# Optimization experiments

Hardware: AMD Instinct MI355X
Metric: run time of the kernel (lower is better)

## Reference

```python
import jax, jax.numpy as jnp
import numpy as np

B = 256          # batch
MID = 16384      # mid_siz
OUT = 16384      # out_siz
C = 16           # channel_siz
NLVL = 8         # nlvl (== klvl here since floor(log2(OUT/2))=13 >= 8)
MIDF = MID >> NLVL   # mid_filter_siz = 64
OUTF = OUT >> NLVL   # out_filter_siz = 64
NB = 1 << NLVL       # 256 leaf branches
STD = 0.5


def setup_inputs() -> dict:
    key = jax.random.key(0)
    ks = jax.random.split(key, 6)
    in_data = jax.random.normal(ks[0], (B, MID, 2), jnp.float32)
    # learned parameters (buildRand: normal(0, 0.5) filters, zero biases)
    mid_dense = jax.random.normal(ks[1], (1, MID, 2), jnp.float32) * STD
    in_filter = jax.random.normal(ks[2], (MIDF, 1, C), jnp.float32) * STD   # conv1d [width,in,out]
    in_bias = jnp.zeros((C,), jnp.float32)
    # level lvl (1..NLVL) uses filters[lvl-1, :2**lvl]; padded to NB branches
    filters = jax.random.normal(ks[3], (NLVL, NB, 2, C, C), jnp.float32) * STD
    biases = jnp.zeros((NLVL, NB, C), jnp.float32)
    fea_dense = jax.random.normal(ks[4], (NB, C, OUTF), jnp.float32) * STD
    return dict(in_data=in_data, mid_dense=mid_dense, in_filter=in_filter,
                in_bias=in_bias, filters=filters, biases=biases, fea_dense=fea_dense)


def reference(in_data, mid_dense, in_filter, in_bias, filters, biases, fea_dense):
    # elementwise modulation then split real/imag channels: (B, 2, MID)
    x = jnp.moveaxis(in_data * mid_dense, -1, 1)
    # level-0 conv1d: kernel MIDF, stride MIDF//2 -> overlapping half-windows.
    # Split signal into half-width chunks h; window t = [h[t], h[t+1]].
    half = MIDF // 2
    h = x.reshape(B, 2, MID // half, half)                 # (B,2,512,32)
    W1 = in_filter[:half, 0, :]                            # (32,C)
    W2 = in_filter[half:, 0, :]
    s = jnp.einsum('bisw,wc->bisc', h[:, :, :-1], W1) \
        + jnp.einsum('bisw,wc->bisc', h[:, :, 1:], W2)
    s = jax.nn.relu(s + in_bias)                           # (B,2,2^(n+1)-1,C)
    state = s[:, :, None]                                  # (B,2,nb=1,L,C)
    # butterfly tree: each level doubles branches; conv kernel=2, stride=2, VALID
    for lvl in range(1, NLVL + 1):
        nb = 1 << lvl
        p = jnp.repeat(state, 2, axis=2)                   # child itk <- parent itk//2
        L = p.shape[3]                                     # odd: 2^(n+1-lvl+1)-1
        xw = p[:, :, :, :L - 1, :].reshape(B, 2, nb, (L - 1) // 2, 2, C)
        W = filters[lvl - 1, :nb]                          # (nb,2,C,C)
        bb = biases[lvl - 1, :nb]                          # (nb,C)
        state = jax.nn.relu(
            jnp.einsum('bintkc,nkcd->bintd', xw, W) + bb[None, None, :, None, :])
    feat = state[:, :, :, 0, :]                            # (B,2,NB,C): L==1 at last level
    outp = jnp.einsum('binc,ncf->binf', feat, fea_dense)   # per-branch dense projection
    R = outp[:, 0].reshape(B, OUT // 2, 2)
    I = outp[:, 1].reshape(B, OUT // 2, 2)
    out_data = ((R[:, :, 0] - I[:, :, 1]) / MID).reshape(B, OUT // 2, 1)
    return out_data, R[:, :, 1]
```

## Files before the change

kernel.cpp:

```cpp
#include <hip/hip_runtime.h>
#include <hip/hip_bf16.h>


#define OUT_HALF 2097152

typedef __attribute__((ext_vector_type(4))) float f32x4;
typedef __attribute__((ext_vector_type(8))) short s16x8;

__device__ __forceinline__ uint fsw(uint a) {
    return a ^ ((((a >> 6) ^ (a >> 8)) & 3u) << 4);
}
__device__ __forceinline__ ushort bfr(float f) {
    __hip_bfloat16 h = __float2bfloat16(f);
    union { __hip_bfloat16 h; ushort u; } cv; cv.h = h; return cv.u;
}
__device__ __forceinline__ uint pk(float a, float b) {
    return (uint)bfr(a) | ((uint)bfr(b) << 16);
}

__device__ __forceinline__ void tree_level(
    char* smb, const int lane, const int wave,
    uint AOff, uint NOff, int lgR, int lgNP, int nTiles,
    uint WOff, int wnb, uint LBOff, int bnb)
{
    const int m  = lane & 15;
    const int kg = lane >> 4;
    const int lgTPP = lgR - 4;
    for (int at = wave; at < nTiles; at += 4) {
        const int p  = at >> lgTPP;
        const int tc = at & ((1 << lgTPP) - 1);
        const int np = p & ((1 << lgNP) - 1);
        const int ii = p >> lgNP;
        s16x8 af = *(const s16x8*)(smb + AOff + (p << (lgR + 6)) +
                                   fsw((uint)((tc * 16 + m) * 64 + kg * 16)));
#pragma unroll
        for (int sib = 0; sib < 2; sib++) {
            const int nl = 2 * np + sib;
            s16x8 bf = *(const s16x8*)(smb + WOff +
                         fsw((uint)((wnb + nl) * 1024 + m * 64 + kg * 16)));
            float bv = *(const float*)(smb + LBOff + ((bnb + nl) * 16 + m) * 4);
            f32x4 acc = {bv, bv, bv, bv};
            acc = __builtin_amdgcn_mfma_f32_16x16x32_bf16(af, bf, acc, 0, 0, 0);
            const int p2 = (ii << (lgNP + 1)) + nl;
            const uint wb = NOff + (p2 << (lgR + 5));
            const int r2 = tc * 8 + kg * 2;
            *(uint*)(smb + wb + fsw((uint)(r2 * 64 + m * 4))) =
                pk(fmaxf(acc.x, 0.f), fmaxf(acc.y, 0.f));
            *(uint*)(smb + wb + fsw((uint)((r2 + 1) * 64 + m * 4))) =
                pk(fmaxf(acc.z, 0.f), fmaxf(acc.w, 0.f));
        }
    }
}

__global__ __launch_bounds__(256, 4)
void ibf_A(const float* __restrict__ in_data, const float* __restrict__ mid_dense,
           const float* __restrict__ in_filter, const float* __restrict__ in_bias,
           const float* __restrict__ filters, const float* __restrict__ biases,
           uint* __restrict__ S3)
{
    __shared__ __align__(16) char smb[29760];
    const int tid = threadIdx.x, lane = tid & 63, wave = tid >> 6;
    const int b = blockIdx.x;
    const int th = blockIdx.y >> 1;
    const int i  = blockIdx.y & 1;

    {
        const float4* inb = (const float4*)in_data + (size_t)b * 8192 + th * 2048;
        const float4* mdb = (const float4*)mid_dense + th * 2048;
        for (int mp = tid; mp < 2064; mp += 256) {
            float4 iv = inb[mp], mv = mdb[mp];
            float xa = i ? iv.y * mv.y : iv.x * mv.x;
            float xb = i ? iv.w * mv.w : iv.z * mv.z;
            *(uint*)(smb + fsw((uint)(mp * 4))) = pk(xa, xb);
        }
    }
    for (int t = tid; t < 3584; t += 256) {
        int nidx = t >> 8, r = t & 255, d = r & 15, c = r >> 4;
        int lvl = (nidx < 2) ? 1 : ((nidx < 6) ? 2 : 3);
        int n = nidx - ((1 << lvl) - 2);
        const float* src = filters + (size_t)(lvl - 1) * 131072 + n * 512 + c * 16 + d;
        *(uint*)(smb + 12416 + fsw((uint)(nidx * 1024 + d * 64 + c * 4))) = pk(src[0], src[256]);
    }
    for (int t = tid; t < 512; t += 256) {
        int c = t >> 5, w2 = t & 31;
        *(uint*)(smb + 26752 + fsw((uint)(c * 128 + w2 * 4))) =
            pk(in_filter[(2 * w2) * 16 + c], in_filter[(2 * w2 + 1) * 16 + c]);
    }
    if (tid < 240) {
        float v;
        if (tid < 224) {
            int nidx = tid >> 4;
            int lvl = (nidx < 2) ? 1 : ((nidx < 6) ? 2 : 3);
            int n = nidx - ((1 << lvl) - 2);
            v = biases[(size_t)(lvl - 1) * 4096 + n * 16 + (tid & 15)];
        } else v = in_bias[tid - 224];
        *(float*)(smb + 28800 + tid * 4) = v;
    }
    __syncthreads();

    {
        const int m = lane & 15, kg = lane >> 4;
        s16x8 b0 = *(const s16x8*)(smb + 26752 + fsw((uint)(m * 128 + kg * 16)));
        s16x8 b1 = *(const s16x8*)(smb + 26752 + fsw((uint)(m * 128 + 64 + kg * 16)));
        float bv = *(const float*)(smb + 28800 + (224 + m) * 4);
        for (int at = wave; at < 8; at += 4) {
            int tc = at;
            s16x8 a0 = *(const s16x8*)(smb + fsw((uint)((tc * 16 + m) * 64 + kg * 16)));
            s16x8 a1 = *(const s16x8*)(smb + fsw((uint)((tc * 16 + m) * 64 + 64 + kg * 16)));
            f32x4 acc = {bv, bv, bv, bv};
            acc = __builtin_amdgcn_mfma_f32_16x16x32_bf16(a0, b0, acc, 0, 0, 0);
            acc = __builtin_amdgcn_mfma_f32_16x16x32_bf16(a1, b1, acc, 0, 0, 0);
            int r2 = tc * 8 + kg * 2;
            *(uint*)(smb + 8320 + fsw((uint)(r2 * 64 + m * 4))) =
                pk(fmaxf(acc.x, 0.f), fmaxf(acc.y, 0.f));
            *(uint*)(smb + 8320 + fsw((uint)((r2 + 1) * 64 + m * 4))) =
                pk(fmaxf(acc.z, 0.f), fmaxf(acc.w, 0.f));
        }
    }
    __syncthreads();
    tree_level(smb, lane, wave, 8320, 0,    6, 0, 4, 12416, 0, 28800, 0);
    __syncthreads();
    tree_level(smb, lane, wave, 0,    8320, 5, 1, 4, 12416, 2, 28800, 2);
    __syncthreads();
    {
        const int m = lane & 15, kg = lane >> 4;
        for (int at = wave; at < 4; at += 4) {
            s16x8 af = *(const s16x8*)(smb + 8320 + (at << 10) + fsw((uint)(m * 64 + kg * 16)));
#pragma unroll
            for (int sib = 0; sib < 2; sib++) {
                int n3 = 2 * at + sib;
                s16x8 bf = *(const s16x8*)(smb + 12416 +
                             fsw((uint)((6 + n3) * 1024 + m * 64 + kg * 16)));
                float bv = *(const float*)(smb + 28800 + ((6 + n3) * 16 + m) * 4);
                f32x4 acc = {bv, bv, bv, bv};
                acc = __builtin_amdgcn_mfma_f32_16x16x32_bf16(af, bf, acc, 0, 0, 0);
                int bi = 2 * b + i;
                int t4 = th * 8 + kg * 2;
                uint idx = ((uint)(n3 * 512 + bi) * 16 + t4) * 16 + m;
                S3[idx]      = pk(fmaxf(acc.x, 0.f), fmaxf(acc.y, 0.f));
                S3[idx + 16] = pk(fmaxf(acc.z, 0.f), fmaxf(acc.w, 0.f));
            }
        }
    }
}

__global__ __launch_bounds__(256, 2)
void ibf_BC(const float* __restrict__ filters, const float* __restrict__ biases,
            const float* __restrict__ fea_dense, const uint* __restrict__ S3,
            float* __restrict__ out)
{
    __shared__ __align__(16) char smb[33536];
    const int tid = threadIdx.x, lane = tid & 63, wave = tid >> 6;
    const int n3 = blockIdx.x, chunk = blockIdx.y;
    const int m = lane & 15, kg = lane >> 4;

    for (int o = tid * 16; o < 16384; o += 4096)
        *(float4*)(smb + 16384 + o) = make_float4(0.f, 0.f, 0.f, 0.f);

    const float* FB1 = filters + (size_t)3 * 131072 + ((size_t)(n3 << 1)) * 512;
    const float* FB2 = filters + (size_t)4 * 131072 + ((size_t)(n3 << 2)) * 512;
    const float* FB3 = filters + (size_t)5 * 131072 + ((size_t)(n3 << 3)) * 512;
    const float* FB4 = filters + (size_t)6 * 131072 + ((size_t)(n3 << 4)) * 512;
    const float* FB5 = filters + (size_t)7 * 131072 + ((size_t)(n3 << 5)) * 512;
    const float* BB1 = biases + (size_t)3 * 4096 + (n3 << 1) * 16;
    const float* BB2 = biases + (size_t)4 * 4096 + (n3 << 2) * 16;
    const float* BB3 = biases + (size_t)5 * 4096 + (n3 << 3) * 16;
    const float* BB4 = biases + (size_t)6 * 4096 + (n3 << 4) * 16;
    const float* BB5 = biases + (size_t)7 * 4096 + (n3 << 5) * 16;

#define LDFRAG(dst, fb, nl)                                                  \
    {                                                                        \
        const float* s_ = (fb) + (nl) * 512 + m;                             \
        _Pragma("unroll")                                                    \
        for (int c4 = 0; c4 < 4; c4++) {                                     \
            int c_ = kg * 4 + c4;                                            \
            (&(dst).x)[c4] = pk(s_[c_ * 16], s_[256 + c_ * 16]);             \
        }                                                                    \
    }

    uint4 f4[2], f5[4];
    float b4[2], b5[4];
    LDFRAG(f4[0], FB1, 0); LDFRAG(f4[1], FB1, 1);
    b4[0] = BB1[m]; b4[1] = BB1[16 + m];
#pragma unroll
    for (int s = 0; s < 4; s++) { LDFRAG(f5[s], FB2, s); b5[s] = BB2[s * 16 + m]; }
    {
        const char* src = (const char*)S3 + ((size_t)n3 * 512 + chunk * 8) * 1024;
        for (int ci = tid; ci < 512; ci += 256)
            *(float4*)(smb + fsw((uint)(ci * 16))) = *(const float4*)(src + ci * 16);
    }
    __syncthreads();

    uint4 f6[4];
    float b6[4];
    {
        const int n0 = (wave >> 1) * 2;
        LDFRAG(f6[0], FB3, n0);     b6[0] = BB3[(n0) * 16 + m];
        LDFRAG(f6[1], FB3, n0 + 1); b6[1] = BB3[(n0 + 1) * 16 + m];
        LDFRAG(f6[2], FB3, n0 + 4); b6[2] = BB3[(n0 + 4) * 16 + m];
        LDFRAG(f6[3], FB3, n0 + 5); b6[3] = BB3[(n0 + 5) * 16 + m];
    }
#pragma unroll
    for (int t2 = 0; t2 < 2; t2++) {
        const int tc = wave + t2 * 4;
        s16x8 af = *(const s16x8*)(smb + fsw((uint)((tc * 16 + m) * 64 + kg * 16)));
#pragma unroll
        for (int sib = 0; sib < 2; sib++) {
            f32x4 acc = {b4[sib], b4[sib], b4[sib], b4[sib]};
            acc = __builtin_amdgcn_mfma_f32_16x16x32_bf16(af, *(const s16x8*)&f4[sib], acc, 0, 0, 0);
            const uint wb = 8192u + (uint)sib * 4096u;
            const int r2 = tc * 8 + kg * 2;
            *(uint*)(smb + wb + fsw((uint)(r2 * 64 + m * 4))) = pk(fmaxf(acc.x, 0.f), fmaxf(acc.y, 0.f));
            *(uint*)(smb + wb + fsw((uint)((r2 + 1) * 64 + m * 4))) = pk(fmaxf(acc.z, 0.f), fmaxf(acc.w, 0.f));
        }
    }
    __syncthreads();

    uint4 f7[4];
    float b7[4];
    {
        LDFRAG(f7[0], FB4, 2 * wave);     b7[0] = BB4[(2 * wave) * 16 + m];
        LDFRAG(f7[1], FB4, 2 * wave + 1); b7[1] = BB4[(2 * wave + 1) * 16 + m];
        LDFRAG(f7[2], FB4, 2 * wave + 8); b7[2] = BB4[(2 * wave + 8) * 16 + m];
        LDFRAG(f7[3], FB4, 2 * wave + 9); b7[3] = BB4[(2 * wave + 9) * 16 + m];
    }
#pragma unroll
    for (int t2 = 0; t2 < 2; t2++) {
        const int at = wave + t2 * 4;
        const int p = at >> 2, tc = at & 3;
        s16x8 af = *(const s16x8*)(smb + 8192 + p * 4096 + fsw((uint)((tc * 16 + m) * 64 + kg * 16)));
#pragma unroll
        for (int sib = 0; sib < 2; sib++) {
            const int nl = 2 * p + sib;
            f32x4 acc = {b5[nl], b5[nl], b5[nl], b5[nl]};
            acc = __builtin_amdgcn_mfma_f32_16x16x32_bf16(af, *(const s16x8*)&f5[nl], acc, 0, 0, 0);
            const uint wb = (uint)nl * 2048u;
            const int r2 = tc * 8 + kg * 2;
            *(uint*)(smb + wb + fsw((uint)(r2 * 64 + m * 4))) = pk(fmaxf(acc.x, 0.f), fmaxf(acc.y, 0.f));
            *(uint*)(smb + wb + fsw((uint)((r2 + 1) * 64 + m * 4))) = pk(fmaxf(acc.z, 0.f), fmaxf(acc.w, 0.f));
        }
    }
    __syncthreads();

    uint4 f8[8];
    float b8[8];
#pragma unroll
    for (int t4 = 0; t4 < 4; t4++) {
        const int at = wave + 4 * t4;
        LDFRAG(f8[2 * t4],     FB5, 2 * at);     b8[2 * t4]     = BB5[(2 * at) * 16 + m];
        LDFRAG(f8[2 * t4 + 1], FB5, 2 * at + 1); b8[2 * t4 + 1] = BB5[(2 * at + 1) * 16 + m];
    }
#pragma unroll
    for (int t2 = 0; t2 < 2; t2++) {
        const int at = wave + t2 * 4;
        const int p = at >> 1, tc = at & 1;
        s16x8 af = *(const s16x8*)(smb + p * 2048 + fsw((uint)((tc * 16 + m) * 64 + kg * 16)));
#pragma unroll
        for (int sib = 0; sib < 2; sib++) {
            const int nl = 2 * p + sib;
            const int fi = t2 * 2 + sib;
            f32x4 acc = {b6[fi], b6[fi], b6[fi], b6[fi]};
            acc = __builtin_amdgcn_mfma_f32_16x16x32_bf16(af, *(const s16x8*)&f6[fi], acc, 0, 0, 0);
            const uint wb = 8192u + (uint)nl * 1024u;
            const int r2 = tc * 8 + kg * 2;
            *(uint*)(smb + wb + fsw((uint)(r2 * 64 + m * 4))) = pk(fmaxf(acc.x, 0.f), fmaxf(acc.y, 0.f));
            *(uint*)(smb + wb + fsw((uint)((r2 + 1) * 64 + m * 4))) = pk(fmaxf(acc.z, 0.f), fmaxf(acc.w, 0.f));
        }
    }
    __syncthreads();

#pragma unroll
    for (int t2 = 0; t2 < 2; t2++) {
        const int p = wave + t2 * 4;
        s16x8 af = *(const s16x8*)(smb + 8192 + p * 1024 + fsw((uint)(m * 64 + kg * 16)));
#pragma unroll
        for (int sib = 0; sib < 2; sib++) {
            const int nl = 2 * p + sib;
            const int fi = t2 * 2 + sib;
            f32x4 acc = {b7[fi], b7[fi], b7[fi], b7[fi]};
            acc = __builtin_amdgcn_mfma_f32_16x16x32_bf16(af, *(const s16x8*)&f7[fi], acc, 0, 0, 0);
            const uint wb = (uint)nl * 512u;
            const int r2 = kg * 2;
            *(uint*)(smb + wb + fsw((uint)(r2 * 64 + m * 4))) = pk(fmaxf(acc.x, 0.f), fmaxf(acc.y, 0.f));
            *(uint*)(smb + wb + fsw((uint)((r2 + 1) * 64 + m * 4))) = pk(fmaxf(acc.z, 0.f), fmaxf(acc.w, 0.f));
        }
    }
    __syncthreads();

#pragma unroll
    for (int t4 = 0; t4 < 4; t4++) {
        const int at = wave + 4 * t4;
        s16x8 af = *(const s16x8*)(smb + at * 512 + fsw((uint)(m * 64 + kg * 16)));
#pragma unroll
        for (int sib = 0; sib < 2; sib++) {
            const int nl = 2 * at + sib;
            const int fi = t4 * 2 + sib;
            f32x4 acc = {b8[fi], b8[fi], b8[fi], b8[fi]};
            acc = __builtin_amdgcn_mfma_f32_16x16x32_bf16(af, *(const s16x8*)&f8[fi], acc, 0, 0, 0);
            if (kg < 2) {
                float v[4] = {fmaxf(acc.x, 0.f), fmaxf(acc.y, 0.f),
                              fmaxf(acc.z, 0.f), fmaxf(acc.w, 0.f)};
#pragma unroll
                for (int j = 0; j < 4; j++) {
                    uint o = (uint)(nl * 512 + (kg * 4 + j) * 64 + m * 2);
                    *(ushort*)(smb + 16384 + fsw(o)) = bfr(v[j]);
                }
            }
        }
    }
    __syncthreads();

    for (int q = 0; q < 8; q++) {
        int n8l = wave * 8 + q;
        int gn8 = n3 * 32 + n8l;
        s16x8 af = *(const s16x8*)(smb + 16384 +
                     fsw((uint)(n8l * 512 + m * 64 + kg * 16)));
        const float* fb = fea_dense + (size_t)gn8 * 1024;
#pragma unroll
        for (int ut = 0; ut < 4; ut++) {
            s16x8 bf = {0, 0, 0, 0, 0, 0, 0, 0};
            if (kg < 2) {
                const float* fp = fb + kg * 512 + ut * 16 + m;
                bf[0] = (short)bfr(fp[0]);   bf[1] = (short)bfr(fp[64]);
                bf[2] = (short)bfr(fp[128]); bf[3] = (short)bfr(fp[192]);
                bf[4] = (short)bfr(fp[256]); bf[5] = (short)bfr(fp[320]);
                bf[6] = (short)bfr(fp[384]); bf[7] = (short)bfr(fp[448]);
            }
            f32x4 acc = {0.f, 0.f, 0.f, 0.f};
            acc = __builtin_amdgcn_mfma_f32_16x16x32_bf16(af, bf, acc, 0, 0, 0);
            float s0 = __shfl_xor(acc.y, 1);
            float s2 = __shfl_xor(acc.w, 1);
            if (kg < 2) {
                int g = gn8 * 32 + ut * 8 + (m >> 1);
                bool odd = (m & 1);
                float v0 = odd ? acc.x : (acc.x - s0) * (1.f / 16384.f);
                float v1 = odd ? acc.z : (acc.z - s2) * (1.f / 16384.f);
                size_t off = (odd ? (size_t)OUT_HALF : (size_t)0) + (size_t)g;
                int b0 = chunk * 4 + kg * 2;
                out[(size_t)b0 * 8192 + off]       = v0;
                out[(size_t)(b0 + 1) * 8192 + off] = v1;
            }
        }
    }
#undef LDFRAG
}

extern "C" void kernel_launch(void* const* d_in, const int* in_sizes, int n_in,
                              void* d_out, int out_size, void* d_ws, size_t ws_size,
                              hipStream_t stream) {
    const float* in_data   = (const float*)d_in[0];
    const float* mid_dense = (const float*)d_in[1];
    const float* in_filter = (const float*)d_in[2];
    const float* in_bias   = (const float*)d_in[3];
    const float* filters   = (const float*)d_in[4];
    const float* biases    = (const float*)d_in[5];
    const float* fea_dense = (const float*)d_in[6];
    float* out = (float*)d_out;
    uint* S3   = (uint*)d_ws;

    ibf_A<<<dim3(256, 4), 256, 0, stream>>>(in_data, mid_dense, in_filter, in_bias,
                                            filters, biases, S3);
    ibf_BC<<<dim3(8, 64), 256, 0, stream>>>(filters, biases, fea_dense, S3, out);
}
```

Baseline: 40.70 us.

## Vectorize filter staging, prefetch fea_dense in registers, reorder S3 load, use dynamic LDS

Filter staging in the first kernel now loads float4 vectors and packs four bf16 pairs per thread instead of scalar gathers. In the second kernel, the S3 tile copy is issued first. The final projection double-buffers fea_dense values in registers so global loads for the next branch overlap the current MFMA work. Shared memory becomes a dynamically sized extern buffer. This raises register pressure, since 64 floats are prefetched per lane, which may hurt occupancy.

```diff
diff --git a/kernel.cpp b/kernel.cpp
--- a/kernel.cpp
+++ b/kernel.cpp
@@ -6,6 +6,8 @@
 
 typedef __attribute__((ext_vector_type(4))) float f32x4;
 typedef __attribute__((ext_vector_type(8))) short s16x8;
+
+extern __shared__ char smb[];
 
 __device__ __forceinline__ uint fsw(uint a) {
     return a ^ ((((a >> 6) ^ (a >> 8)) & 3u) << 4);
@@ -19,7 +21,7 @@
 }
 
 __device__ __forceinline__ void tree_level(
-    char* smb, const int lane, const int wave,
+    const int lane, const int wave,
     uint AOff, uint NOff, int lgR, int lgNP, int nTiles,
     uint WOff, int wnb, uint LBOff, int bnb)
 {
@@ -58,7 +60,6 @@
            const float* __restrict__ filters, const float* __restrict__ biases,
            uint* __restrict__ S3)
 {
-    __shared__ __align__(16) char smb[29760];
     const int tid = threadIdx.x, lane = tid & 63, wave = tid >> 6;
     const int b = blockIdx.x;
     const int th = blockIdx.y >> 1;
@@ -74,12 +75,20 @@
             *(uint*)(smb + fsw((uint)(mp * 4))) = pk(xa, xb);
         }
     }
-    for (int t = tid; t < 3584; t += 256) {
-        int nidx = t >> 8, r = t & 255, d = r & 15, c = r >> 4;
+    for (int t = tid; t < 896; t += 256) {
+        int nidx = t >> 6, r = t & 63, c = r >> 2, d4 = (r & 3) * 4;
         int lvl = (nidx < 2) ? 1 : ((nidx < 6) ? 2 : 3);
         int n = nidx - ((1 << lvl) - 2);
-        const float* src = filters + (size_t)(lvl - 1) * 131072 + n * 512 + c * 16 + d;
-        *(uint*)(smb + 12416 + fsw((uint)(nidx * 1024 + d * 64 + c * 4))) = pk(src[0], src[256]);
+        const float* src = filters + (size_t)(lvl - 1) * 131072 + n * 512 + c * 16 + d4;
+        float4 v0 = *(const float4*)(src);
+        float4 v1 = *(const float4*)(src + 256);
+        const float* p0 = &v0.x;
+        const float* p1 = &v1.x;
+#pragma unroll
+        for (int j = 0; j < 4; j++) {
+            *(uint*)(smb + 12416 + fsw((uint)(nidx * 1024 + (d4 + j) * 64 + c * 4))) =
+                pk(p0[j], p1[j]);
+        }
     }
     for (int t = tid; t < 512; t += 256) {
         int c = t >> 5, w2 = t & 31;
@@ -118,9 +127,9 @@
         }
     }
     __syncthreads();
-    tree_level(smb, lane, wave, 8320, 0,    6, 0, 4, 12416, 0, 28800, 0);
-    __syncthreads();
-    tree_level(smb, lane, wave, 0,    8320, 5, 1, 4, 12416, 2, 28800, 2);
+    tree_level(lane, wave, 8320, 0,    6, 0, 4, 12416, 0, 28800, 0);
+    __syncthreads();
+    tree_level(lane, wave, 0,    8320, 5, 1, 4, 12416, 2, 28800, 2);
     __syncthreads();
     {
         const int m = lane & 15, kg = lane >> 4;
@@ -149,11 +158,15 @@
             const float* __restrict__ fea_dense, const uint* __restrict__ S3,
             float* __restrict__ out)
 {
-    __shared__ __align__(16) char smb[33536];
     const int tid = threadIdx.x, lane = tid & 63, wave = tid >> 6;
     const int n3 = blockIdx.x, chunk = blockIdx.y;
     const int m = lane & 15, kg = lane >> 4;
 
+    {
+        const char* src = (const char*)S3 + ((size_t)n3 * 512 + chunk * 8) * 1024;
+        for (int ci = tid; ci < 512; ci += 256)
+            *(float4*)(smb + fsw((uint)(ci * 16))) = *(const float4*)(src + ci * 16);
+    }
     for (int o = tid * 16; o < 16384; o += 4096)
         *(float4*)(smb + 16384 + o) = make_float4(0.f, 0.f, 0.f, 0.f);
 
@@ -184,11 +197,6 @@
     b4[0] = BB1[m]; b4[1] = BB1[16 + m];
 #pragma unroll
     for (int s = 0; s < 4; s++) { LDFRAG(f5[s], FB2, s); b5[s] = BB2[s * 16 + m]; }
-    {
-        const char* src = (const char*)S3 + ((size_t)n3 * 512 + chunk * 8) * 1024;
-        for (int ci = tid; ci < 512; ci += 256)
-            *(float4*)(smb + fsw((uint)(ci * 16))) = *(const float4*)(src + ci * 16);
-    }
     __syncthreads();
 
     uint4 f6[4];
@@ -310,35 +318,54 @@
     }
     __syncthreads();
 
-    for (int q = 0; q < 8; q++) {
-        int n8l = wave * 8 + q;
-        int gn8 = n3 * 32 + n8l;
-        s16x8 af = *(const s16x8*)(smb + 16384 +
-                     fsw((uint)(n8l * 512 + m * 64 + kg * 16)));
-        const float* fb = fea_dense + (size_t)gn8 * 1024;
-#pragma unroll
-        for (int ut = 0; ut < 4; ut++) {
-            s16x8 bf = {0, 0, 0, 0, 0, 0, 0, 0};
-            if (kg < 2) {
-                const float* fp = fb + kg * 512 + ut * 16 + m;
-                bf[0] = (short)bfr(fp[0]);   bf[1] = (short)bfr(fp[64]);
-                bf[2] = (short)bfr(fp[128]); bf[3] = (short)bfr(fp[192]);
-                bf[4] = (short)bfr(fp[256]); bf[5] = (short)bfr(fp[320]);
-                bf[6] = (short)bfr(fp[384]); bf[7] = (short)bfr(fp[448]);
+    {
+        float feA[32], feB[32];
+        const float* fbase = fea_dense + (size_t)(n3 * 32 + wave * 8) * 1024 + kg * 512 + m;
+        if (kg < 2) {
+#pragma unroll
+            for (int ut = 0; ut < 4; ut++)
+#pragma unroll
+                for (int j = 0; j < 8; j++)
+                    feA[ut * 8 + j] = fbase[ut * 16 + j * 64];
+        }
+#pragma unroll
+        for (int q = 0; q < 8; q++) {
+            float* cur = (q & 1) ? feB : feA;
+            float* nxt = (q & 1) ? feA : feB;
+            if (q < 7 && kg < 2) {
+                const float* fn = fbase + (size_t)(q + 1) * 1024;
+#pragma unroll
+                for (int ut = 0; ut < 4; ut++)
+#pragma unroll
+                    for (int j = 0; j < 8; j++)
+                        nxt[ut * 8 + j] = fn[ut * 16 + j * 64];
             }
-            f32x4 acc = {0.f, 0.f, 0.f, 0.f};
-            acc = __builtin_amdgcn_mfma_f32_16x16x32_bf16(af, bf, acc, 0, 0, 0);
-            float s0 = __shfl_xor(acc.y, 1);
-            float s2 = __shfl_xor(acc.w, 1);
-            if (kg < 2) {
-                int g = gn8 * 32 + ut * 8 + (m >> 1);
-                bool odd = (m & 1);
-                float v0 = odd ? acc.x : (acc.x - s0) * (1.f / 16384.f);
-                float v1 = odd ? acc.z : (acc.z - s2) * (1.f / 16384.f);
-                size_t off = (odd ? (size_t)OUT_HALF : (size_t)0) + (size_t)g;
-                int b0 = chunk * 4 + kg * 2;
-                out[(size_t)b0 * 8192 + off]       = v0;
-                out[(size_t)(b0 + 1) * 8192 + off] = v1;
+            const int n8l = wave * 8 + q;
+            const int gn8 = n3 * 32 + n8l;
+            s16x8 af = *(const s16x8*)(smb + 16384 +
+                         fsw((uint)(n8l * 512 + m * 64 + kg * 16)));
+#pragma unroll
+            for (int ut = 0; ut < 4; ut++) {
+                s16x8 bf = {0, 0, 0, 0, 0, 0, 0, 0};
+                if (kg < 2) {
+#pragma unroll
+                    for (int j = 0; j < 8; j++)
+                        bf[j] = (short)bfr(cur[ut * 8 + j]);
+                }
+                f32x4 acc = {0.f, 0.f, 0.f, 0.f};
+                acc = __builtin_amdgcn_mfma_f32_16x16x32_bf16(af, bf, acc, 0, 0, 0);
+                float s0 = __shfl_xor(acc.y, 1);
+                float s2 = __shfl_xor(acc.w, 1);
+                if (kg < 2) {
+                    int g = gn8 * 32 + ut * 8 + (m >> 1);
+                    bool odd = (m & 1);
+                    float v0 = odd ? acc.x : (acc.x - s0) * (1.f / 16384.f);
+                    float v1 = odd ? acc.z : (acc.z - s2) * (1.f / 16384.f);
+                    size_t off = (odd ? (size_t)OUT_HALF : (size_t)0) + (size_t)g;
+                    int b0 = chunk * 4 + kg * 2;
+                    out[(size_t)b0 * 8192 + off]       = v0;
+                    out[(size_t)(b0 + 1) * 8192 + off] = v1;
+                }
             }
         }
     }
@@ -358,7 +385,7 @@
     float* out = (float*)d_out;
     uint* S3   = (uint*)d_ws;
 
-    ibf_A<<<dim3(256, 4), 256, 0, stream>>>(in_data, mid_dense, in_filter, in_bias,
-                                            filters, biases, S3);
-    ibf_BC<<<dim3(8, 64), 256, 0, stream>>>(filters, biases, fea_dense, S3, out);
-}
+    ibf_A<<<dim3(256, 4), 256, 29760, stream>>>(in_data, mid_dense, in_filter, in_bias,
+                                                filters, biases, S3);
+    ibf_BC<<<dim3(8, 64), 256, 33536, stream>>>(filters, biases, fea_dense, S3, out);
+}
```

Result: faster. 37.98 us (-6.7%).
